# Optimization experiments

Hardware: AMD Instinct MI355X
Metric: run time of the kernel (lower is better)

The kernel has to match this reference:

```python
import jax, jax.numpy as jnp
import numpy as np

B, S, D, H, WS = 2, 4096, 768, 12, 256
HD = D // H
NW = S // WS
EPS = 1e-5


def layernorm(x, g, b):
    mu = jnp.mean(x, axis=-1, keepdims=True)
    var = jnp.mean(jnp.square(x - mu), axis=-1, keepdims=True)
    return (x - mu) * jax.lax.rsqrt(var + EPS) * g + b


def setup_inputs() -> dict:
    key = jax.random.key(0)
    ks = jax.random.split(key, 8)
    s = 0.02
    return {
        "x": jax.random.normal(ks[0], (B, S, D), dtype=jnp.float32),
        "Wq": jax.random.normal(ks[1], (D, D), dtype=jnp.float32) * s,
        "bq": jnp.zeros((D,), jnp.float32),
        "Wk": jax.random.normal(ks[2], (D, D), dtype=jnp.float32) * s,
        "bk": jnp.zeros((D,), jnp.float32),
        "Wv": jax.random.normal(ks[3], (D, D), dtype=jnp.float32) * s,
        "bv": jnp.zeros((D,), jnp.float32),
        "Wo": jax.random.normal(ks[4], (D, D), dtype=jnp.float32) * s,
        "bo": jnp.zeros((D,), jnp.float32),
        "ln1_g": jnp.ones((D,), jnp.float32),
        "ln1_b": jnp.zeros((D,), jnp.float32),
        "W1": jax.random.normal(ks[5], (D, 4 * D), dtype=jnp.float32) * s,
        "b1": jnp.zeros((4 * D,), jnp.float32),
        "W2": jax.random.normal(ks[6], (4 * D, D), dtype=jnp.float32) * s,
        "b2": jnp.zeros((D,), jnp.float32),
        "ln2_g": jnp.ones((D,), jnp.float32),
        "ln2_b": jnp.zeros((D,), jnp.float32),
    }


def _attn(h, Wq, bq, Wk, bk, Wv, bv, Wo, bo):
    q = (h @ Wq + bq).reshape(B, S, H, HD)
    k = (h @ Wk + bk).reshape(B, S, H, HD)
    v = (h @ Wv + bv).reshape(B, S, H, HD)
    # split into windows: [B, NW, WS, H, HD]
    kb = k.reshape(B, NW, WS, H, HD)
    vb = v.reshape(B, NW, WS, H, HD)
    qw = jnp.moveaxis(q.reshape(B, NW, WS, H, HD), 1, 0)  # [NW, B, WS, H, HD]
    inv = 1.0 / np.sqrt(HD).astype(np.float32)

    def step(carry, qi_i):
        qi, i = qi_i  # qi: [B, WS, H, HD]
        # per key-window scores: [B, H, NW, WSq, WSk]
        scores = jnp.einsum('bqhd,bjkhd->bhjqk', qi, kb) * inv
        attn = jax.nn.softmax(scores, axis=-1)  # per-block softmax (as in source)
        mask = (jnp.arange(NW) <= i).astype(attn.dtype)  # block-causal, include own window
        attn = attn * mask[None, None, :, None, None]
        ctx = jnp.einsum('bhjqk,bjkhd->bqhd', attn, vb)  # sum over key windows
        return carry, ctx

    _, ctxs = jax.lax.scan(step, None, (qw, jnp.arange(NW)))
    ctx = jnp.moveaxis(ctxs, 0, 1).reshape(B, S, D)
    return ctx @ Wo + bo


def reference(x, Wq, bq, Wk, bk, Wv, bv, Wo, bo, ln1_g, ln1_b, W1, b1, W2, b2, ln2_g, ln2_b):
    attn_out = _attn(layernorm(x, ln1_g, ln1_b), Wq, bq, Wk, bk, Wv, bv, Wo, bo)
    x = x + attn_out
    h2 = layernorm(x, ln2_g, ln2_b)
    ff = jax.nn.gelu(h2 @ W1 + b1, approximate=False) @ W2 + b2
    return x + ff
```

## Files before the change

### kernel.cpp

```cpp
#include <hip/hip_runtime.h>
#include <cstdint>
#include <cstddef>

#define DEV __device__ __forceinline__

typedef unsigned short u16;
typedef unsigned int u32;
typedef __attribute__((ext_vector_type(8))) short s16x8;
typedef __attribute__((ext_vector_type(4))) float f32x4;
typedef __attribute__((ext_vector_type(4))) unsigned int u32x4;

typedef unsigned int u32_as1 __attribute__((address_space(1)));
typedef unsigned int u32_as3 __attribute__((address_space(3)));

DEV u16 f2bf(float f){
  unsigned u = __float_as_uint(f);
  u += 0x7fffu + ((u >> 16) & 1u);
  return (u16)(u >> 16);
}

DEV float bf2f(u16 v){ return __uint_as_float(((u32)v) << 16); }

DEV u32 cvtpk_bf16(float lo, float hi){
  u32 r;
  asm("v_cvt_pk_bf16_f32 %0, %1, %2" : "=v"(r) : "v"(lo), "v"(hi));
  return r;
}

DEV float fexp2(float x){
  float r;
  asm("v_exp_f32 %0, %1" : "=v"(r) : "v"(x));
  return r;
}

DEV float frcp(float x){
  float r;
  asm("v_rcp_f32 %0, %1" : "=v"(r) : "v"(x));
  return r;
}

DEV void gload16(const void* g, void* l){
  __builtin_amdgcn_global_load_lds((const u32_as1*)g, (u32_as3*)l, 16, 0, 0);
}

DEV float gelu_tanh(float x){
  float x2 = x*x;
  float z = 2.3022083f * x * fmaf(x2, 0.044715f, 1.0f);
  z = fminf(z, 100.0f);
  float t = fexp2(z);
  return x * t * frcp(t + 1.0f);
}

template<int NZ>
__global__ __launch_bounds__(256) void wconv_kernel(
    const float* __restrict__ Wa, const float* __restrict__ Wb,
    const float* __restrict__ Wc, const float* __restrict__ Wd,
    u16* __restrict__ Da, u16* __restrict__ Db, u16* __restrict__ Dc, u16* __restrict__ Dd,
    int K, int N){
  __shared__ float tl[32][33];
  int z = (NZ>1) ? blockIdx.z : 0;
  const float* W = (z==0)?Wa:(z==1)?Wb:(z==2)?Wc:Wd;
  u16* Wt = (z==0)?Da:(z==1)?Db:(z==2)?Dc:Dd;
  int tx = threadIdx.x & 31, ty = threadIdx.x >> 5;
  int k0 = blockIdx.x * 32, n0 = blockIdx.y * 32;
  #pragma unroll
  for (int p=0;p<4;p++)
    tl[ty+8*p][tx] = W[(size_t)(k0+ty+8*p)*N + (n0+tx)];
  __syncthreads();
  #pragma unroll
  for (int p=0;p<4;p++){
    int n = ty+8*p;
    Wt[(size_t)(n0+n)*K + (k0+tx)] = f2bf(tl[tx][n]);
  }
}

template<bool INBF16>
__global__ __launch_bounds__(256) void ln_kernel(const void* __restrict__ xin,
                                                 const float* __restrict__ g,
                                                 const float* __restrict__ bta,
                                                 u16* __restrict__ out){
  int row = blockIdx.x, t = threadIdx.x;
  float v0, v1, v2;
  if (INBF16){
    const u16* xr = (const u16*)xin + (size_t)row*768;
    v0 = bf2f(xr[t]); v1 = bf2f(xr[t+256]); v2 = bf2f(xr[t+512]);
  } else {
    const float* xr = (const float*)xin + (size_t)row*768;
    v0 = xr[t]; v1 = xr[t+256]; v2 = xr[t+512];
  }
  float s = v0+v1+v2, s2 = v0*v0+v1*v1+v2*v2;
  #pragma unroll
  for (int m=1;m<64;m<<=1){ s += __shfl_xor(s,m); s2 += __shfl_xor(s2,m); }
  __shared__ float ls[4], ls2[4];
  int w = t>>6;
  if ((t&63)==0){ ls[w]=s; ls2[w]=s2; }
  __syncthreads();
  s = ls[0]+ls[1]+ls[2]+ls[3]; s2 = ls2[0]+ls2[1]+ls2[2]+ls2[3];
  float mu = s*(1.0f/768.0f);
  float rstd = rsqrtf(s2*(1.0f/768.0f) - mu*mu + 1e-5f);
  u16* orow = out + (size_t)row*768;
  orow[t]     = f2bf((v0-mu)*rstd*g[t]     + bta[t]);
  orow[t+256] = f2bf((v1-mu)*rstd*g[t+256] + bta[t+256]);
  orow[t+512] = f2bf((v2-mu)*rstd*g[t+512] + bta[t+512]);
}

template<bool GELU, bool RES, bool OUTBF16, int BM, bool VPERM=false, bool RESBF16=false>
__global__ __launch_bounds__(256) void gemm_kernel(
    const u16* __restrict__ A, const u16* __restrict__ Bt0, size_t btStride,
    const float* __restrict__ bias0, const float* __restrict__ bias1, const float* __restrict__ bias2,
    const void* __restrict__ res, void* __restrict__ out0, size_t outStride,
    int M, int N, int K, float qscale, u32* __restrict__ vtb = nullptr)
{
  constexpr int AM = BM/32;
  __shared__ u16 As[BM*64];
  __shared__ u16 Bs[128*64];
  const int t = threadIdx.x, lane = t & 63, w = t >> 6;
  const int lj = lane & 15, g = lane >> 4;
  const int wm = w >> 1, wn = w & 1;
  const int z = blockIdx.z;
  const u16* Bt = Bt0 + (size_t)z * btStride;
  const float* bias = (z==0) ? bias0 : (z==1 ? bias1 : bias2);
  const u16* Arow = A  + (size_t)blockIdx.x * BM * K;
  const u16* Brow = Bt + (size_t)blockIdx.y * 128 * K;

  f32x4 acc[AM][4];
  #pragma unroll
  for (int a=0;a<AM;a++)
    #pragma unroll
    for (int b=0;b<4;b++){ f32x4 zz = {0.f,0.f,0.f,0.f}; acc[a][b] = zz; }

  for (int kk=0; kk<K; kk+=64){
    #pragma unroll
    for (int cc=0;cc<BM/32;cc++){
      int c = cc*256 + t;
      int row = c>>3, gp = c&7;
      gload16(Arow + (size_t)row*K + kk + ((gp ^ (row&7))<<3),
              (void*)(As + (size_t)(cc*256 + w*64)*8));
    }
    #pragma unroll
    for (int cc=0;cc<4;cc++){
      int c = cc*256 + t;
      int row = c>>3, gp = c&7;
      gload16(Brow + (size_t)row*K + kk + ((gp ^ (row&7))<<3),
              (void*)(Bs + (size_t)(cc*256 + w*64)*8));
    }
    __syncthreads();
    #pragma unroll
    for (int ks=0;ks<2;ks++){
      s16x8 af[AM], bfr[4];
      #pragma unroll
      for (int mt=0;mt<AM;mt++){
        int row = wm*(BM/2)+mt*16+lj;
        af[mt]  = *(const s16x8*)&As[(size_t)row*64 + (((ks*4+g) ^ (lj&7))<<3)];
      }
      #pragma unroll
      for (int nt=0;nt<4;nt++){
        int row = wn*64+nt*16+lj;
        bfr[nt] = *(const s16x8*)&Bs[(size_t)row*64 + (((ks*4+g) ^ (lj&7))<<3)];
      }
      #pragma unroll
      for (int mt=0;mt<AM;mt++)
        #pragma unroll
        for (int nt=0;nt<4;nt++)
          acc[mt][nt] = __builtin_amdgcn_mfma_f32_16x16x32_bf16(af[mt], bfr[nt], acc[mt][nt], 0,0,0);
    }
    __syncthreads();
  }

  const size_t gr0 = (size_t)blockIdx.x*BM + wm*(BM/2);
  const int gc0 = blockIdx.y*128 + wn*64;

  if (VPERM && z == 2){
    const int b_ = (int)(gr0 >> 12);
    const int kt = (int)((gr0 & 4095) >> 6);
    #pragma unroll
    for (int mt2=0; mt2<AM; mt2+=2){
      const u32 gnq = 4*(mt2>>1) + g;
      #pragma unroll
      for (int nt=0;nt<4;nt++){
        int gc = gc0 + nt*16 + lj;
        int hh = gc>>6, dd = gc&63;
        float bv = bias[gc];
        size_t base = ((size_t)(b_*12+hh)*64 + dd)*2048 + (size_t)kt*32 + gnq*4;
        #pragma unroll
        for (int r=0;r<4;r++){
          float ve = acc[mt2][nt][r]   + bv;
          float vo = acc[mt2+1][nt][r] + bv;
          vtb[base + r] = cvtpk_bf16(ve, vo);
        }
      }
    }
    return;
  }

  float* outF = (float*)out0; u16* outB = (u16*)out0;
  if (OUTBF16) outB += (size_t)z*outStride; else outF += (size_t)z*outStride;
  #pragma unroll
  for (int mt=0;mt<AM;mt++)
    #pragma unroll
    for (int nt=0;nt<4;nt++){
      int gc = gc0 + nt*16 + lj;
      float bv = bias[gc];
      #pragma unroll
      for (int r=0;r<4;r++){
        size_t gr = gr0 + mt*16 + g*4 + r;
        float val = acc[mt][nt][r] + bv;
        if (z==0) val *= qscale;
        if (RES){
          if (RESBF16) val += bf2f(((const u16*)res)[gr*(size_t)N + gc]);
          else         val += ((const float*)res)[gr*(size_t)N + gc];
        }
        if (GELU) val = gelu_tanh(val);
        if (OUTBF16) outB[gr*(size_t)N + gc] = f2bf(val);
        else         outF[gr*(size_t)N + gc] = val;
      }
    }
}

__global__ __launch_bounds__(256,3) void attn_kernel(
    const u16* __restrict__ qb, const u16* __restrict__ kb,
    const u16* __restrict__ vtb, u16* __restrict__ ctx)
{
  __shared__ u16 KV[256*64];
  const int t = threadIdx.x, lane = t & 63, w = t >> 6;
  const int lj = lane & 15, g = lane >> 4;
  const int bx = blockIdx.x;
  const int pp = bx & 7, qq = (bx >> 3) & 3, bh = bx >> 5;
  const int h = bh % 12, b = bh / 12;
  const size_t seqbase = (size_t)b * 4096;
  const int hoff = h * 64;

  #pragma unroll
  for (int f=0; f<2; f++){
    const int iw = f ? (15 - pp) : pp;
    const int qrow0 = iw*256 + qq*64 + w*16;

    s16x8 qa[2];
    #pragma unroll
    for (int ks=0;ks<2;ks++)
      qa[ks] = *(const s16x8*)(qb + (seqbase + qrow0 + lj)*768 + hoff + ks*32 + g*8);

    f32x4 cacc[4];
    #pragma unroll
    for (int dt=0;dt<4;dt++){ f32x4 zz = {0.f,0.f,0.f,0.f}; cacc[dt] = zz; }

    for (int jw=0; jw<=iw; jw++){
      const u16* kwin = kb + (seqbase + jw*256)*768 + hoff;
      const u16* vtwin = vtb + (size_t)bh*64*4096 + jw*256;

      __syncthreads();
      #pragma unroll
      for (int cc=0;cc<8;cc++){
        int c = cc*256 + t;
        int krow = c>>3, vp = c&7;
        gload16(kwin + (size_t)krow*768 + ((vp ^ (krow&7))<<3),
                (void*)(KV + (size_t)(cc*256 + w*64)*8));
      }
      __syncthreads();

      f32x4 sacc[16];
      #pragma unroll
      for (int kt=0;kt<16;kt++){ f32x4 zz = {0.f,0.f,0.f,0.f}; sacc[kt] = zz; }
      __builtin_amdgcn_s_setprio(1);
      #pragma unroll
      for (int kt=0;kt<16;kt++){
        int kl = kt*16 + lj;
        #pragma unroll
        for (int ks=0;ks<2;ks++){
          s16x8 kf = *(const s16x8*)&KV[ (size_t)kl*64 + (((4*ks+g) ^ (kl&7))<<3) ];
          sacc[kt] = __builtin_amdgcn_mfma_f32_16x16x32_bf16(kf, qa[ks], sacc[kt], 0,0,0);
        }
      }
      __builtin_amdgcn_s_setprio(0);
      __syncthreads();

      #pragma unroll
      for (int cc=0;cc<8;cc++){
        int c = cc*256 + t;
        int d = c>>5, cp = c&31;
        gload16(vtwin + (size_t)d*4096 + ((cp ^ (d&15))<<3),
                (void*)(KV + (size_t)(cc*256 + w*64)*8));
      }

      float sm = 0.f;
      #pragma unroll
      for (int kt=0;kt<16;kt++)
        #pragma unroll
        for (int r=0;r<4;r++){
          float pv = fexp2(sacc[kt][r]);
          sacc[kt][r] = pv; sm += pv;
        }
      sm += __shfl_xor(sm, 16);
      sm += __shfl_xor(sm, 32);
      float rs = frcp(sm);

      __syncthreads();

      f32x4 pacc[4];
      #pragma unroll
      for (int dt=0;dt<4;dt++){ f32x4 zz = {0.f,0.f,0.f,0.f}; pacc[dt] = zz; }
      #pragma unroll
      for (int ks=0;ks<8;ks++){
        u32x4 pw;
        #pragma unroll
        for (int r=0;r<4;r++)
          pw[r] = cvtpk_bf16(sacc[2*ks][r], sacc[2*ks+1][r]);
        s16x8 pa = __builtin_bit_cast(s16x8, pw);
        __builtin_amdgcn_s_setprio(1);
        #pragma unroll
        for (int dt=0;dt<4;dt++){
          int d = dt*16 + lj;
          s16x8 vf = *(const s16x8*)&KV[ (size_t)d*256 + (((4*ks+g) ^ (d&15))<<3) ];
          pacc[dt] = __builtin_amdgcn_mfma_f32_16x16x32_bf16(pa, vf, pacc[dt], 0,0,0);
        }
        __builtin_amdgcn_s_setprio(0);
      }
      #pragma unroll
      for (int dt=0;dt<4;dt++)
        #pragma unroll
        for (int r=0;r<4;r++)
          cacc[dt][r] += rs * pacc[dt][r];
    }

    #pragma unroll
    for (int dt=0;dt<4;dt++)
      #pragma unroll
      for (int r=0;r<4;r++){
        int qrow = qrow0 + g*4 + r;
        ctx[ (seqbase + qrow)*768 + hoff + dt*16 + lj ] = f2bf(cacc[dt][r]);
      }
  }
}

extern "C" void kernel_launch(void* const* d_in, const int* in_sizes, int n_in,
                              void* d_out, int out_size, void* d_ws, size_t ws_size,
                              hipStream_t stream)
{
  const float* x    = (const float*)d_in[0];
  const float* Wq   = (const float*)d_in[1];
  const float* bq   = (const float*)d_in[2];
  const float* Wk   = (const float*)d_in[3];
  const float* bk   = (const float*)d_in[4];
  const float* Wv   = (const float*)d_in[5];
  const float* bv   = (const float*)d_in[6];
  const float* Wo   = (const float*)d_in[7];
  const float* bo   = (const float*)d_in[8];
  const float* ln1g = (const float*)d_in[9];
  const float* ln1b = (const float*)d_in[10];
  const float* W1   = (const float*)d_in[11];
  const float* b1   = (const float*)d_in[12];
  const float* W2   = (const float*)d_in[13];
  const float* b2   = (const float*)d_in[14];
  const float* ln2g = (const float*)d_in[15];
  const float* ln2b = (const float*)d_in[16];

  char* ws = (char*)d_ws;
  constexpr size_t SZ_W768  = (size_t)768*768*2;
  constexpr size_t SZ_W3072 = (size_t)768*3072*2;
  constexpr size_t SZ_HB    = (size_t)8192*768*2;
  u16* wtq = (u16*)(ws);
  u16* wtk = (u16*)(ws + SZ_W768);
  u16* wtv = (u16*)(ws + 2*SZ_W768);
  u16* wto = (u16*)(ws + 3*SZ_W768);
  u16* wt1 = (u16*)(ws + 4*SZ_W768);
  u16* wt2 = (u16*)(ws + 4*SZ_W768 + SZ_W3072);
  char* p0 = ws + 4*SZ_W768 + 2*SZ_W3072;
  u16*   hbuf  = (u16*)p0;
  u16*   qbuf  = (u16*)(p0 + SZ_HB);
  u16*   kbuf  = (u16*)(p0 + 2*SZ_HB);
  u16*   vtbuf = (u16*)(p0 + 3*SZ_HB);
  u16*   cbuf  = (u16*)(p0 + 4*SZ_HB);
  u16*   x1    = (u16*)(p0 + 5*SZ_HB);
  u16*   ffa   = qbuf;
  float* outp  = (float*)d_out;

  wconv_kernel<4><<<dim3(24,24,4), 256, 0, stream>>>(
      Wq, Wk, Wv, Wo, wtq, wtk, wtv, wto, 768, 768);
  wconv_kernel<1><<<dim3(24,96), 256, 0, stream>>>(
      W1, W1, W1, W1, wt1, wt1, wt1, wt1, 768, 3072);
  wconv_kernel<1><<<dim3(96,24), 256, 0, stream>>>(
      W2, W2, W2, W2, wt2, wt2, wt2, wt2, 3072, 768);

  ln_kernel<false><<<8192, 256, 0, stream>>>(x, ln1g, ln1b, hbuf);
  gemm_kernel<false,false,true,128,true><<<dim3(64,6,3), 256, 0, stream>>>(
      hbuf, wtq, (size_t)768*768, bq, bk, bv, nullptr, qbuf, (size_t)8192*768,
      8192, 768, 768, 0.180336880111f, (u32*)vtbuf);
  attn_kernel<<<768, 256, 0, stream>>>(qbuf, kbuf, vtbuf, cbuf);
  gemm_kernel<false,true,true,64><<<dim3(128,6,1), 256, 0, stream>>>(
      cbuf, wto, 0, bo, bo, bo, x, x1, 0, 8192, 768, 768, 1.0f);
  ln_kernel<true><<<8192, 256, 0, stream>>>(x1, ln2g, ln2b, hbuf);
  gemm_kernel<true,false,true,128><<<dim3(64,24,1), 256, 0, stream>>>(
      hbuf, wt1, 0, b1, b1, b1, nullptr, ffa, 0, 8192, 3072, 768, 1.0f);
  gemm_kernel<false,true,false,64,false,true><<<dim3(128,6,1), 256, 0, stream>>>(
      ffa, wt2, 0, b2, b2, b2, x1, outp, 0, 8192, 768, 3072, 1.0f);
}
```

Before: 275.8 us.

## Rewrite windowed attention with 32x32 MFMA and split V staging

The attention kernel moves from 16x16x32 to 32x32x16 bf16 MFMA tiles, with each wave handling 32 query rows. Scores are exponentiated and fed straight into the PV product per 32-key tile, so the 16 score accumulators are no longer held live. K and V now sit in separate LDS buffers, and V is staged in two 128-key halves. The V-transpose epilogue of the projection GEMM is changed to write the permuted layout that the 32x32 operand needs. Work is redistributed as one query half-window per block, ordered from the longest causal window first, which drops the earlier pairing of long and short windows and may cost load balance. Keeping K and V resident together also raises LDS use per block.

After: 286.2 us. 1.04x slower.

```diff
diff --git a/kernel.cpp b/kernel.cpp
--- a/kernel.cpp
+++ b/kernel.cpp
@@ -8,7 +8,9 @@
 typedef unsigned int u32;
 typedef __attribute__((ext_vector_type(8))) short s16x8;
 typedef __attribute__((ext_vector_type(4))) float f32x4;
+typedef __attribute__((ext_vector_type(16))) float f32x16;
 typedef __attribute__((ext_vector_type(4))) unsigned int u32x4;
+typedef __attribute__((ext_vector_type(2))) unsigned int u32x2;
 
 typedef unsigned int u32_as1 __attribute__((address_space(1)));
 typedef unsigned int u32_as3 __attribute__((address_space(3)));
@@ -37,6 +39,13 @@
   float r;
   asm("v_rcp_f32 %0, %1" : "=v"(r) : "v"(x));
   return r;
+}
+
+DEV f32x16 zero16(){
+  f32x16 z;
+  #pragma unroll
+  for (int i=0;i<16;i++) z[i] = 0.f;
+  return z;
 }
 
 DEV void gload16(const void* g, void* l){
@@ -172,22 +181,20 @@
 
   if (VPERM && z == 2){
     const int b_ = (int)(gr0 >> 12);
-    const int kt = (int)((gr0 & 4095) >> 6);
-    #pragma unroll
-    for (int mt2=0; mt2<AM; mt2+=2){
-      const u32 gnq = 4*(mt2>>1) + g;
+    const int kt64 = (int)((gr0 & 4095) >> 6);
+    #pragma unroll
+    for (int mt=0; mt<AM; mt++){
       #pragma unroll
       for (int nt=0;nt<4;nt++){
         int gc = gc0 + nt*16 + lj;
         int hh = gc>>6, dd = gc&63;
         float bv = bias[gc];
-        size_t base = ((size_t)(b_*12+hh)*64 + dd)*2048 + (size_t)kt*32 + gnq*4;
-        #pragma unroll
-        for (int r=0;r<4;r++){
-          float ve = acc[mt2][nt][r]   + bv;
-          float vo = acc[mt2+1][nt][r] + bv;
-          vtb[base + r] = cvtpk_bf16(ve, vo);
-        }
+        size_t base = (((size_t)(b_*12+hh)*64 + dd)*4096 + (size_t)kt64*64)/2
+                      + (size_t)(mt*8 + ((g&1)<<2) + ((g>>1)<<1));
+        u32x2 wv;
+        wv[0] = cvtpk_bf16(acc[mt][nt][0]+bv, acc[mt][nt][1]+bv);
+        wv[1] = cvtpk_bf16(acc[mt][nt][2]+bv, acc[mt][nt][3]+bv);
+        *(u32x2*)(vtb + base) = wv;
       }
     }
     return;
@@ -221,114 +228,114 @@
     const u16* __restrict__ qb, const u16* __restrict__ kb,
     const u16* __restrict__ vtb, u16* __restrict__ ctx)
 {
-  __shared__ u16 KV[256*64];
+  __shared__ u16 Ks[256*64];
+  __shared__ u16 Vs[64*128];
   const int t = threadIdx.x, lane = t & 63, w = t >> 6;
-  const int lj = lane & 15, g = lane >> 4;
+  const int l31 = lane & 31, hi = lane >> 5;
   const int bx = blockIdx.x;
-  const int pp = bx & 7, qq = (bx >> 3) & 3, bh = bx >> 5;
+  const int iw = 15 - (bx / 48);
+  const int r48 = bx - (bx / 48) * 48;
+  const int bh = r48 >> 1, qh = r48 & 1;
   const int h = bh % 12, b = bh / 12;
   const size_t seqbase = (size_t)b * 4096;
   const int hoff = h * 64;
-
-  #pragma unroll
-  for (int f=0; f<2; f++){
-    const int iw = f ? (15 - pp) : pp;
-    const int qrow0 = iw*256 + qq*64 + w*16;
-
-    s16x8 qa[2];
-    #pragma unroll
-    for (int ks=0;ks<2;ks++)
-      qa[ks] = *(const s16x8*)(qb + (seqbase + qrow0 + lj)*768 + hoff + ks*32 + g*8);
-
-    f32x4 cacc[4];
-    #pragma unroll
-    for (int dt=0;dt<4;dt++){ f32x4 zz = {0.f,0.f,0.f,0.f}; cacc[dt] = zz; }
-
-    for (int jw=0; jw<=iw; jw++){
-      const u16* kwin = kb + (seqbase + jw*256)*768 + hoff;
-      const u16* vtwin = vtb + (size_t)bh*64*4096 + jw*256;
-
-      __syncthreads();
-      #pragma unroll
-      for (int cc=0;cc<8;cc++){
-        int c = cc*256 + t;
-        int krow = c>>3, vp = c&7;
-        gload16(kwin + (size_t)krow*768 + ((vp ^ (krow&7))<<3),
-                (void*)(KV + (size_t)(cc*256 + w*64)*8));
-      }
-      __syncthreads();
-
-      f32x4 sacc[16];
-      #pragma unroll
-      for (int kt=0;kt<16;kt++){ f32x4 zz = {0.f,0.f,0.f,0.f}; sacc[kt] = zz; }
-      __builtin_amdgcn_s_setprio(1);
-      #pragma unroll
-      for (int kt=0;kt<16;kt++){
-        int kl = kt*16 + lj;
+  const int qrow0 = iw*256 + qh*128 + w*32;
+
+  s16x8 qa[4];
+  #pragma unroll
+  for (int ksl=0; ksl<4; ksl++)
+    qa[ksl] = *(const s16x8*)(qb + (seqbase + qrow0 + l31)*768 + hoff + ksl*16 + hi*8);
+
+  f32x16 cacc0 = zero16(), cacc1 = zero16();
+
+  for (int jw=0; jw<=iw; ++jw){
+    const u16* kwin  = kb  + (seqbase + jw*256)*768 + hoff;
+    const u16* vtwin = vtb + (size_t)bh*64*4096 + jw*256;
+
+    __syncthreads();
+    #pragma unroll
+    for (int cc=0;cc<8;cc++){
+      int c = cc*256 + t;
+      int kl = c>>3, gp = c&7;
+      gload16(kwin + (size_t)kl*768 + ((gp ^ (kl&7))<<3),
+              (void*)(Ks + (size_t)(cc*256 + w*64)*8));
+    }
+    #pragma unroll
+    for (int cc=0;cc<4;cc++){
+      int c = cc*256 + t;
+      int d = c>>4, gp = c&15;
+      gload16(vtwin + (size_t)d*4096 + ((gp ^ (d&15))<<3),
+              (void*)(Vs + (size_t)(cc*256 + w*64)*8));
+    }
+    __syncthreads();
+
+    f32x16 pacc0 = zero16(), pacc1 = zero16();
+    float sm = 0.f;
+    #pragma unroll
+    for (int half=0; half<2; ++half){
+      if (half){
+        __syncthreads();
         #pragma unroll
-        for (int ks=0;ks<2;ks++){
-          s16x8 kf = *(const s16x8*)&KV[ (size_t)kl*64 + (((4*ks+g) ^ (kl&7))<<3) ];
-          sacc[kt] = __builtin_amdgcn_mfma_f32_16x16x32_bf16(kf, qa[ks], sacc[kt], 0,0,0);
+        for (int cc=0;cc<4;cc++){
+          int c = cc*256 + t;
+          int d = c>>4, gp = c&15;
+          gload16(vtwin + (size_t)d*4096 + 128 + ((gp ^ (d&15))<<3),
+                  (void*)(Vs + (size_t)(cc*256 + w*64)*8));
         }
-      }
-      __builtin_amdgcn_s_setprio(0);
-      __syncthreads();
-
-      #pragma unroll
-      for (int cc=0;cc<8;cc++){
-        int c = cc*256 + t;
-        int d = c>>5, cp = c&31;
-        gload16(vtwin + (size_t)d*4096 + ((cp ^ (d&15))<<3),
-                (void*)(KV + (size_t)(cc*256 + w*64)*8));
-      }
-
-      float sm = 0.f;
-      #pragma unroll
-      for (int kt=0;kt<16;kt++)
-        #pragma unroll
-        for (int r=0;r<4;r++){
-          float pv = fexp2(sacc[kt][r]);
-          sacc[kt][r] = pv; sm += pv;
-        }
-      sm += __shfl_xor(sm, 16);
-      sm += __shfl_xor(sm, 32);
-      float rs = frcp(sm);
-
-      __syncthreads();
-
-      f32x4 pacc[4];
-      #pragma unroll
-      for (int dt=0;dt<4;dt++){ f32x4 zz = {0.f,0.f,0.f,0.f}; pacc[dt] = zz; }
-      #pragma unroll
-      for (int ks=0;ks<8;ks++){
-        u32x4 pw;
-        #pragma unroll
-        for (int r=0;r<4;r++)
-          pw[r] = cvtpk_bf16(sacc[2*ks][r], sacc[2*ks+1][r]);
-        s16x8 pa = __builtin_bit_cast(s16x8, pw);
+        __syncthreads();
+      }
+      #pragma unroll
+      for (int kt4=0; kt4<4; ++kt4){
+        const int kt = half*4 + kt4;
+        const int kl = kt*32 + l31;
+        f32x16 sacc = zero16();
         __builtin_amdgcn_s_setprio(1);
         #pragma unroll
-        for (int dt=0;dt<4;dt++){
-          int d = dt*16 + lj;
-          s16x8 vf = *(const s16x8*)&KV[ (size_t)d*256 + (((4*ks+g) ^ (d&15))<<3) ];
-          pacc[dt] = __builtin_amdgcn_mfma_f32_16x16x32_bf16(pa, vf, pacc[dt], 0,0,0);
+        for (int ksl=0; ksl<4; ++ksl){
+          s16x8 kf = *(const s16x8*)&Ks[(size_t)kl*64 + (((ksl*2+hi) ^ (kl&7))<<3)];
+          sacc = __builtin_amdgcn_mfma_f32_32x32x16_bf16(kf, qa[ksl], sacc, 0,0,0);
         }
         __builtin_amdgcn_s_setprio(0);
-      }
-      #pragma unroll
-      for (int dt=0;dt<4;dt++)
+        u32 pw[8];
         #pragma unroll
-        for (int r=0;r<4;r++)
-          cacc[dt][r] += rs * pacc[dt][r];
-    }
-
-    #pragma unroll
-    for (int dt=0;dt<4;dt++)
-      #pragma unroll
-      for (int r=0;r<4;r++){
-        int qrow = qrow0 + g*4 + r;
-        ctx[ (seqbase + qrow)*768 + hoff + dt*16 + lj ] = f2bf(cacc[dt][r]);
-      }
+        for (int j=0;j<8;j++){
+          float e0 = fexp2(sacc[2*j]);
+          float e1 = fexp2(sacc[2*j+1]);
+          sm += e0 + e1;
+          pw[j] = cvtpk_bf16(e0, e1);
+        }
+        #pragma unroll
+        for (int s=0;s<2;s++){
+          u32x4 w4 = { pw[4*s], pw[4*s+1], pw[4*s+2], pw[4*s+3] };
+          s16x8 pa = __builtin_bit_cast(s16x8, w4);
+          __builtin_amdgcn_s_setprio(1);
+          #pragma unroll
+          for (int dt=0;dt<2;dt++){
+            int d = dt*32 + l31;
+            int gi = (kt4*4 + s*2 + hi) ^ (d&15);
+            s16x8 vf = *(const s16x8*)&Vs[(size_t)d*128 + (gi<<3)];
+            if (dt==0) pacc0 = __builtin_amdgcn_mfma_f32_32x32x16_bf16(pa, vf, pacc0, 0,0,0);
+            else       pacc1 = __builtin_amdgcn_mfma_f32_32x32x16_bf16(pa, vf, pacc1, 0,0,0);
+          }
+          __builtin_amdgcn_s_setprio(0);
+        }
+      }
+    }
+    sm += __shfl_xor(sm, 32);
+    float rs = frcp(sm);
+    #pragma unroll
+    for (int r=0;r<16;r++){
+      cacc0[r] += rs * pacc0[r];
+      cacc1[r] += rs * pacc1[r];
+    }
+  }
+
+  #pragma unroll
+  for (int r=0;r<16;r++){
+    int q = qrow0 + (r&3) + 8*(r>>2) + 4*hi;
+    u16* crow = ctx + (seqbase + q)*768 + hoff;
+    crow[l31]      = f2bf(cacc0[r]);
+    crow[32 + l31] = f2bf(cacc1[r]);
   }
 }
 
```
